# Kernel optimization log

Measured on AMD Instinct MI355X. Metric: run time of the kernel, lower is better.

The kernel has to match this reference:

```python
import jax, jax.numpy as jnp
import numpy as np

B, V_IN, V_OUT, C_IN, C_OUT, SPIRAL, K_NNZ = 4, 12500, 50000, 64, 32, 9, 3

def setup_inputs() -> dict:
    key = jax.random.key(0)
    k1, k2, k3, k4, k5 = jax.random.split(key, 5)
    x = jax.random.normal(k1, (B, V_IN, C_IN), dtype=jnp.float32)
    spiral_indices = jax.random.randint(k2, (V_OUT, SPIRAL), 0, V_OUT)
    up_idx = jax.random.randint(k3, (V_OUT, K_NNZ), 0, V_IN)
    up_val = jax.random.uniform(k4, (V_OUT, K_NNZ), dtype=jnp.float32)
    weight = jax.random.normal(k5, (SPIRAL * C_IN, C_OUT), dtype=jnp.float32) / np.sqrt(SPIRAL * C_IN)
    bias = jnp.zeros((C_OUT,), dtype=jnp.float32)
    return {"x": x, "spiral_indices": spiral_indices, "up_idx": up_idx,
            "up_val": up_val, "weight": weight, "bias": bias}

def reference(x, spiral_indices, up_idx, up_val, weight, bias):
    # pool_bvc: sparse up_transform @ x, 3 nnz per output vertex
    # x: [B, V_in, C]; up_idx/up_val: [V_out, K]
    up = jnp.einsum('bvkc,vk->bvc', x[:, up_idx], up_val)  # [B, V_out, C_in]
    # SpiralConv: gather spiral neighborhoods, flatten, linear
    g = up[:, spiral_indices]                               # [B, V_out, S, C_in]
    g = g.reshape(g.shape[0], g.shape[1], -1)               # [B, V_out, S*C_in]
    y = jnp.einsum('bvf,fo->bvo', g, weight) + bias         # [B, V_out, C_out]
    return jax.nn.relu(y)
```

## Files before the change

### kernel.cpp

```cpp
#include <hip/hip_runtime.h>
#include <hip/hip_bf16.h>

#define B_     4
#define V_IN   12500
#define V_OUT  50000
#define C_IN   64
#define C_OUT  32
#define SPIRAL 9
#define K_NNZ  3
#define ROWS   (B_ * V_OUT)
#define KDIM   (SPIRAL * C_IN)
#define KSTEPS (KDIM / 32)
#define WFRAG_ELEMS (KSTEPS * 2 * 64 * 8)

typedef __attribute__((ext_vector_type(8))) short short8_t;
typedef __attribute__((ext_vector_type(4))) float floatx4;

__device__ __forceinline__ unsigned short f32_to_bf16(float f) {
    unsigned int u = __float_as_uint(f);
    unsigned int r = u + 0x7fffu + ((u >> 16) & 1u);
    return (unsigned short)(r >> 16);
}

__global__ __launch_bounds__(256) void upsample_kernel(
    const float* __restrict__ x,
    const int* __restrict__ up_idx,
    const float* __restrict__ up_val,
    const float* __restrict__ weight,
    unsigned short* __restrict__ up_bf16,
    unsigned short* __restrict__ w_frag)
{
    int tid = threadIdx.x;
    if (blockIdx.x == ROWS / 16) {
        for (int idx = tid; idx < WFRAG_ELEMS; idx += 256) {
            int j     = idx & 7;
            int lane  = (idx >> 3) & 63;
            int ntile = (idx >> 9) & 1;
            int kstep = idx >> 10;
            int k = kstep * 32 + (lane >> 4) * 8 + j;
            int n = ntile * 16 + (lane & 15);
            w_frag[idx] = f32_to_bf16(weight[k * C_OUT + n]);
        }
        return;
    }
    int r      = blockIdx.x * 16 + (tid >> 4);
    int lane16 = tid & 15;
    int b = r / V_OUT;
    int v = r - b * V_OUT;
    const int*   ui = up_idx + v * K_NNZ;
    const float* uv = up_val + v * K_NNZ;
    float a0 = 0.f, a1 = 0.f, a2 = 0.f, a3 = 0.f;
#pragma unroll
    for (int k = 0; k < K_NNZ; k++) {
        int u = ui[k];
        float val = uv[k];
        const float4* xp = (const float4*)(x + ((size_t)b * V_IN + u) * C_IN) + lane16;
        float4 xv = *xp;
        a0 += val * xv.x; a1 += val * xv.y; a2 += val * xv.z; a3 += val * xv.w;
    }
    ushort4 o;
    o.x = f32_to_bf16(a0); o.y = f32_to_bf16(a1);
    o.z = f32_to_bf16(a2); o.w = f32_to_bf16(a3);
    *((ushort4*)(up_bf16 + (size_t)r * C_IN) + lane16) = o;
}

__global__ __launch_bounds__(256) void gemm_kernel(
    const unsigned short* __restrict__ up_bf16,
    const int* __restrict__ spiral,
    const unsigned short* __restrict__ w_frag,
    const float* __restrict__ bias,
    float* __restrict__ out)
{
    __shared__ __align__(16) unsigned short w_lds[WFRAG_ELEMS];
    int tid = threadIdx.x;
    {
        const uint4* src = (const uint4*)w_frag;
        uint4* dst = (uint4*)w_lds;
        for (int i = tid; i < WFRAG_ELEMS / 8; i += 256) dst[i] = src[i];
    }
    __syncthreads();

    int wave = tid >> 6;
    int lane = tid & 63;
    int m    = lane & 15;
    int quad = lane >> 4;

    int r = blockIdx.x * 64 + wave * 16 + m;
    int b = r / V_OUT;
    int v = r - b * V_OUT;

    const int* sp = spiral + v * SPIRAL;
    int su[SPIRAL];
#pragma unroll
    for (int s = 0; s < SPIRAL; s++) su[s] = sp[s];
    size_t base = (size_t)b * V_OUT * C_IN;

    floatx4 acc0 = {0.f, 0.f, 0.f, 0.f};
    floatx4 acc1 = {0.f, 0.f, 0.f, 0.f};

#pragma unroll
    for (int kstep = 0; kstep < KSTEPS; kstep++) {
        int s   = kstep >> 1;
        int off = (kstep & 1) * 32 + quad * 8;
        const short8_t* ap = (const short8_t*)(up_bf16 + base + (size_t)su[s] * C_IN + off);
        short8_t afrag = *ap;
        const short8_t* bp0 = (const short8_t*)(w_lds + ((kstep * 2 + 0) * 64 + lane) * 8);
        const short8_t* bp1 = (const short8_t*)(w_lds + ((kstep * 2 + 1) * 64 + lane) * 8);
        short8_t bfrag0 = *bp0;
        short8_t bfrag1 = *bp1;
        acc0 = __builtin_amdgcn_mfma_f32_16x16x32_bf16(afrag, bfrag0, acc0, 0, 0, 0);
        acc1 = __builtin_amdgcn_mfma_f32_16x16x32_bf16(afrag, bfrag1, acc1, 0, 0, 0);
    }

    float bias0 = bias[m];
    float bias1 = bias[16 + m];
    int row_base = blockIdx.x * 64 + wave * 16 + quad * 4;
#pragma unroll
    for (int reg = 0; reg < 4; reg++) {
        int rr = row_base + reg;
        float y0 = acc0[reg] + bias0; y0 = y0 > 0.f ? y0 : 0.f;
        float y1 = acc1[reg] + bias1; y1 = y1 > 0.f ? y1 : 0.f;
        out[(size_t)rr * C_OUT + m]      = y0;
        out[(size_t)rr * C_OUT + 16 + m] = y1;
    }
}

extern "C" void kernel_launch(void* const* d_in, const int* in_sizes, int n_in,
                              void* d_out, int out_size, void* d_ws, size_t ws_size,
                              hipStream_t stream) {
    const float* x      = (const float*)d_in[0];
    const int*   spiral = (const int*)d_in[1];
    const int*   up_idx = (const int*)d_in[2];
    const float* up_val = (const float*)d_in[3];
    const float* weight = (const float*)d_in[4];
    const float* bias   = (const float*)d_in[5];
    float* out = (float*)d_out;

    unsigned short* up_ws  = (unsigned short*)d_ws;
    unsigned short* w_frag = up_ws + (size_t)ROWS * C_IN;

    upsample_kernel<<<ROWS / 16 + 1, 256, 0, stream>>>(x, up_idx, up_val, weight, up_ws, w_frag);
    gemm_kernel<<<ROWS / 64, 256, 0, stream>>>(up_ws, spiral, w_frag, bias, out);
}
```

Before: 136.6 us.

## Make GEMM persistent, preload gathers, and swap MFMA operands for vector stores

The GEMM kernel becomes a persistent grid of 1024 blocks looping over 64-row tiles, so the weight fragments are copied into LDS once per block instead of once per tile. All 18 spiral-gather loads for a tile are issued before the MFMA chain to raise memory-level parallelism. The MFMA operands are swapped so each lane holds four consecutive output channels, which allows float4 bias loads and float4 output stores instead of scalar ones. The cost is higher register pressure from the preloaded fragments and fewer resident blocks than the original one-block-per-tile launch.

```diff
diff --git a/kernel.cpp b/kernel.cpp
--- a/kernel.cpp
+++ b/kernel.cpp
@@ -11,6 +11,8 @@
 #define ROWS   (B_ * V_OUT)
 #define KDIM   (SPIRAL * C_IN)
 #define KSTEPS (KDIM / 32)
+#define NTILES (ROWS / 64)
+#define GRID2  1024
 #define WFRAG_ELEMS (KSTEPS * 2 * 64 * 8)
 
 typedef __attribute__((ext_vector_type(8))) short short8_t;
@@ -85,43 +87,47 @@
     int m    = lane & 15;
     int quad = lane >> 4;
 
-    int r = blockIdx.x * 64 + wave * 16 + m;
-    int b = r / V_OUT;
-    int v = r - b * V_OUT;
+    float4 bias0 = ((const float4*)bias)[quad];
+    float4 bias1 = ((const float4*)bias)[4 + quad];
 
-    const int* sp = spiral + v * SPIRAL;
-    int su[SPIRAL];
+    for (int tile = blockIdx.x; tile < NTILES; tile += GRID2) {
+        int r = tile * 64 + wave * 16 + m;
+        int b = r / V_OUT;
+        int v = r - b * V_OUT;
+        const int* sp = spiral + v * SPIRAL;
+        size_t base = (size_t)b * V_OUT * C_IN;
+
+        short8_t g0[SPIRAL], g1[SPIRAL];
 #pragma unroll
-    for (int s = 0; s < SPIRAL; s++) su[s] = sp[s];
-    size_t base = (size_t)b * V_OUT * C_IN;
+        for (int s = 0; s < SPIRAL; s++) {
+            const unsigned short* rowp = up_bf16 + base + (size_t)sp[s] * C_IN;
+            g0[s] = *(const short8_t*)(rowp + quad * 8);
+            g1[s] = *(const short8_t*)(rowp + 32 + quad * 8);
+        }
 
-    floatx4 acc0 = {0.f, 0.f, 0.f, 0.f};
-    floatx4 acc1 = {0.f, 0.f, 0.f, 0.f};
+        floatx4 acc0 = {0.f, 0.f, 0.f, 0.f};
+        floatx4 acc1 = {0.f, 0.f, 0.f, 0.f};
+#pragma unroll
+        for (int kstep = 0; kstep < KSTEPS; kstep++) {
+            short8_t gf = (kstep & 1) ? g1[kstep >> 1] : g0[kstep >> 1];
+            const short8_t* wp0 = (const short8_t*)(w_lds + ((kstep * 2 + 0) * 64 + lane) * 8);
+            const short8_t* wp1 = (const short8_t*)(w_lds + ((kstep * 2 + 1) * 64 + lane) * 8);
+            acc0 = __builtin_amdgcn_mfma_f32_16x16x32_bf16(*wp0, gf, acc0, 0, 0, 0);
+            acc1 = __builtin_amdgcn_mfma_f32_16x16x32_bf16(*wp1, gf, acc1, 0, 0, 0);
+        }
 
-#pragma unroll
-    for (int kstep = 0; kstep < KSTEPS; kstep++) {
-        int s   = kstep >> 1;
-        int off = (kstep & 1) * 32 + quad * 8;
-        const short8_t* ap = (const short8_t*)(up_bf16 + base + (size_t)su[s] * C_IN + off);
-        short8_t afrag = *ap;
-        const short8_t* bp0 = (const short8_t*)(w_lds + ((kstep * 2 + 0) * 64 + lane) * 8);
-        const short8_t* bp1 = (const short8_t*)(w_lds + ((kstep * 2 + 1) * 64 + lane) * 8);
-        short8_t bfrag0 = *bp0;
-        short8_t bfrag1 = *bp1;
-        acc0 = __builtin_amdgcn_mfma_f32_16x16x32_bf16(afrag, bfrag0, acc0, 0, 0, 0);
-        acc1 = __builtin_amdgcn_mfma_f32_16x16x32_bf16(afrag, bfrag1, acc1, 0, 0, 0);
-    }
-
-    float bias0 = bias[m];
-    float bias1 = bias[16 + m];
-    int row_base = blockIdx.x * 64 + wave * 16 + quad * 4;
-#pragma unroll
-    for (int reg = 0; reg < 4; reg++) {
-        int rr = row_base + reg;
-        float y0 = acc0[reg] + bias0; y0 = y0 > 0.f ? y0 : 0.f;
-        float y1 = acc1[reg] + bias1; y1 = y1 > 0.f ? y1 : 0.f;
-        out[(size_t)rr * C_OUT + m]      = y0;
-        out[(size_t)rr * C_OUT + 16 + m] = y1;
+        float4 o0, o1;
+        o0.x = acc0[0] + bias0.x; o0.y = acc0[1] + bias0.y;
+        o0.z = acc0[2] + bias0.z; o0.w = acc0[3] + bias0.w;
+        o1.x = acc1[0] + bias1.x; o1.y = acc1[1] + bias1.y;
+        o1.z = acc1[2] + bias1.z; o1.w = acc1[3] + bias1.w;
+        o0.x = o0.x > 0.f ? o0.x : 0.f;  o0.y = o0.y > 0.f ? o0.y : 0.f;
+        o0.z = o0.z > 0.f ? o0.z : 0.f;  o0.w = o0.w > 0.f ? o0.w : 0.f;
+        o1.x = o1.x > 0.f ? o1.x : 0.f;  o1.y = o1.y > 0.f ? o1.y : 0.f;
+        o1.z = o1.z > 0.f ? o1.z : 0.f;  o1.w = o1.w > 0.f ? o1.w : 0.f;
+        float* op = out + (size_t)r * C_OUT;
+        *(float4*)(op + quad * 4)      = o0;
+        *(float4*)(op + 16 + quad * 4) = o1;
     }
 }
 
@@ -140,5 +146,5 @@
     unsigned short* w_frag = up_ws + (size_t)ROWS * C_IN;
 
     upsample_kernel<<<ROWS / 16 + 1, 256, 0, stream>>>(x, up_idx, up_val, weight, up_ws, w_frag);
-    gemm_kernel<<<ROWS / 64, 256, 0, stream>>>(up_ws, spiral, w_frag, bias, out);
+    gemm_kernel<<<GRID2, 256, 0, stream>>>(up_ws, spiral, w_frag, bias, out);
 }
```

New measurement: 139.5 us. 1.02x slower.

## Switch gemm to 32x32x16 MFMA with transposed operands and prefetched spiral gathers

Applied to the files above, without the earlier changes.

The gemm kernel now uses the 32x32x16 bf16 MFMA with the weight as the A operand and gathered rows as B. Each lane owns one output row, so output stores become contiguous float4 writes. Each wave covers 32 rows, and the gathers for the next spiral neighbor are double-buffered in registers so their latency overlaps the MFMAs. Row tiles grow to 128 with a bounds guard. The weight fragment layout is rebuilt to match, and register pressure rises from the 16-wide accumulator plus two gather buffers.

```diff
diff --git a/kernel.cpp b/kernel.cpp
--- a/kernel.cpp
+++ b/kernel.cpp
@@ -10,11 +10,12 @@
 #define K_NNZ  3
 #define ROWS   (B_ * V_OUT)
 #define KDIM   (SPIRAL * C_IN)
-#define KSTEPS (KDIM / 32)
-#define WFRAG_ELEMS (KSTEPS * 2 * 64 * 8)
+#define KSTEPS (KDIM / 16)
+#define TILES  ((ROWS + 127) / 128)
+#define WFRAG_ELEMS (KSTEPS * 64 * 8)
 
-typedef __attribute__((ext_vector_type(8))) short short8_t;
-typedef __attribute__((ext_vector_type(4))) float floatx4;
+typedef __attribute__((ext_vector_type(8)))  short short8_t;
+typedef __attribute__((ext_vector_type(16))) float floatx16;
 
 __device__ __forceinline__ unsigned short f32_to_bf16(float f) {
     unsigned int u = __float_as_uint(f);
@@ -35,10 +36,9 @@
         for (int idx = tid; idx < WFRAG_ELEMS; idx += 256) {
             int j     = idx & 7;
             int lane  = (idx >> 3) & 63;
-            int ntile = (idx >> 9) & 1;
-            int kstep = idx >> 10;
-            int k = kstep * 32 + (lane >> 4) * 8 + j;
-            int n = ntile * 16 + (lane & 15);
+            int kstep = idx >> 9;
+            int k = kstep * 16 + (lane >> 5) * 8 + j;
+            int n = lane & 31;
             w_frag[idx] = f32_to_bf16(weight[k * C_OUT + n]);
         }
         return;
@@ -72,56 +72,73 @@
     float* __restrict__ out)
 {
     __shared__ __align__(16) unsigned short w_lds[WFRAG_ELEMS];
-    int tid = threadIdx.x;
+    int tid  = threadIdx.x;
+    int wave = tid >> 6;
+    int lane = tid & 63;
+    int c32  = lane & 31;
+    int h    = lane >> 5;
+
+    int r = blockIdx.x * 128 + wave * 32 + c32;
+    int valid = r < ROWS;
+    int rs = valid ? r : ROWS - 1;
+    int b = rs / V_OUT;
+    int v = rs - b * V_OUT;
+    const int* sp = spiral + v * SPIRAL;
+    size_t base = (size_t)b * V_OUT * C_IN;
+
     {
         const uint4* src = (const uint4*)w_frag;
         uint4* dst = (uint4*)w_lds;
-        for (int i = tid; i < WFRAG_ELEMS / 8; i += 256) dst[i] = src[i];
+#pragma unroll
+        for (int i = 0; i < WFRAG_ELEMS / 8 / 256; i++)
+            dst[tid + i * 256] = src[tid + i * 256];
     }
     __syncthreads();
 
-    int wave = tid >> 6;
-    int lane = tid & 63;
-    int m    = lane & 15;
-    int quad = lane >> 4;
+    floatx16 acc;
+#pragma unroll
+    for (int i = 0; i < 16; i++) acc[i] = 0.f;
 
-    int r = blockIdx.x * 64 + wave * 16 + m;
-    int b = r / V_OUT;
-    int v = r - b * V_OUT;
-
-    const int* sp = spiral + v * SPIRAL;
-    int su[SPIRAL];
+    short8_t gbuf[2][4];
+    {
+        const unsigned short* rowp = up_bf16 + base + (size_t)sp[0] * C_IN + h * 8;
 #pragma unroll
-    for (int s = 0; s < SPIRAL; s++) su[s] = sp[s];
-    size_t base = (size_t)b * V_OUT * C_IN;
-
-    floatx4 acc0 = {0.f, 0.f, 0.f, 0.f};
-    floatx4 acc1 = {0.f, 0.f, 0.f, 0.f};
-
+        for (int q = 0; q < 4; q++)
+            gbuf[0][q] = *(const short8_t*)(rowp + q * 16);
+    }
 #pragma unroll
-    for (int kstep = 0; kstep < KSTEPS; kstep++) {
-        int s   = kstep >> 1;
-        int off = (kstep & 1) * 32 + quad * 8;
-        const short8_t* ap = (const short8_t*)(up_bf16 + base + (size_t)su[s] * C_IN + off);
-        short8_t afrag = *ap;
-        const short8_t* bp0 = (const short8_t*)(w_lds + ((kstep * 2 + 0) * 64 + lane) * 8);
-        const short8_t* bp1 = (const short8_t*)(w_lds + ((kstep * 2 + 1) * 64 + lane) * 8);
-        short8_t bfrag0 = *bp0;
-        short8_t bfrag1 = *bp1;
-        acc0 = __builtin_amdgcn_mfma_f32_16x16x32_bf16(afrag, bfrag0, acc0, 0, 0, 0);
-        acc1 = __builtin_amdgcn_mfma_f32_16x16x32_bf16(afrag, bfrag1, acc1, 0, 0, 0);
+    for (int s = 0; s < SPIRAL; s++) {
+        int cur = s & 1, nxt = cur ^ 1;
+        if (s + 1 < SPIRAL) {
+            const unsigned short* rowp = up_bf16 + base + (size_t)sp[s + 1] * C_IN + h * 8;
+#pragma unroll
+            for (int q = 0; q < 4; q++)
+                gbuf[nxt][q] = *(const short8_t*)(rowp + q * 16);
+        }
+#pragma unroll
+        for (int q = 0; q < 4; q++) {
+            int kstep = s * 4 + q;
+            const short8_t* wp = (const short8_t*)(w_lds + (kstep * 64 + lane) * 8);
+            acc = __builtin_amdgcn_mfma_f32_32x32x16_bf16(*wp, gbuf[cur][q], acc, 0, 0, 0);
+        }
     }
 
-    float bias0 = bias[m];
-    float bias1 = bias[16 + m];
-    int row_base = blockIdx.x * 64 + wave * 16 + quad * 4;
+    if (valid) {
+        float* op = out + (size_t)r * C_OUT;
 #pragma unroll
-    for (int reg = 0; reg < 4; reg++) {
-        int rr = row_base + reg;
-        float y0 = acc0[reg] + bias0; y0 = y0 > 0.f ? y0 : 0.f;
-        float y1 = acc1[reg] + bias1; y1 = y1 > 0.f ? y1 : 0.f;
-        out[(size_t)rr * C_OUT + m]      = y0;
-        out[(size_t)rr * C_OUT + 16 + m] = y1;
+        for (int g = 0; g < 4; g++) {
+            float4 bv = *(const float4*)(bias + g * 8 + h * 4);
+            float4 o4;
+            o4.x = acc[g * 4 + 0] + bv.x;
+            o4.y = acc[g * 4 + 1] + bv.y;
+            o4.z = acc[g * 4 + 2] + bv.z;
+            o4.w = acc[g * 4 + 3] + bv.w;
+            o4.x = o4.x > 0.f ? o4.x : 0.f;
+            o4.y = o4.y > 0.f ? o4.y : 0.f;
+            o4.z = o4.z > 0.f ? o4.z : 0.f;
+            o4.w = o4.w > 0.f ? o4.w : 0.f;
+            *(float4*)(op + g * 8 + h * 4) = o4;
+        }
     }
 }
 
@@ -140,5 +157,5 @@
     unsigned short* w_frag = up_ws + (size_t)ROWS * C_IN;
 
     upsample_kernel<<<ROWS / 16 + 1, 256, 0, stream>>>(x, up_idx, up_val, weight, up_ws, w_frag);
-    gemm_kernel<<<ROWS / 64, 256, 0, stream>>>(up_ws, spiral, w_frag, bias, out);
+    gemm_kernel<<<TILES, 256, 0, stream>>>(up_ws, spiral, w_frag, bias, out);
 }
```

New measurement: 142.4 us. 1.04x slower.
